# Kernel optimization log

Hardware: AMD Instinct MI355X
Metric: run time of the kernel (lower is better)

Reference implementation:

```python
import math
import jax, jax.numpy as jnp
import numpy as np

NUM_EXPERTS = 8
TOP_K = 2
HIDDEN = 1024
INTER = 4096
CAPACITY_FACTOR = 1.25
S, B = 2048, 4


def setup_inputs() -> dict:
    key = jax.random.key(0)
    k1, k2, k3, k4 = jax.random.split(key, 4)
    hidden_states = jax.random.normal(k1, (S, B, HIDDEN), dtype=jnp.float32)
    T = S * B
    logits = jax.random.normal(k2, (T, NUM_EXPERTS), dtype=jnp.float32)
    expert_affinities = jax.nn.softmax(logits, axis=-1)  # (T, E), normalized per token
    # top-k chosen experts per token (no duplicates), consistent with affinities
    _, expert_index = jax.lax.top_k(expert_affinities, TOP_K)  # (T, top_k) int32
    gate_up_proj = jax.random.normal(k3, (NUM_EXPERTS, HIDDEN, 2 * INTER), dtype=jnp.float32) * 0.02
    down_proj = jax.random.normal(k4, (NUM_EXPERTS, INTER, HIDDEN), dtype=jnp.float32) * 0.02
    return {
        "hidden_states": hidden_states,
        "expert_affinities": expert_affinities,
        "expert_index": expert_index.astype(jnp.int32),
        "gate_up_proj": gate_up_proj,
        "down_proj": down_proj,
    }


def reference(hidden_states, expert_affinities, expert_index, gate_up_proj, down_proj):
    S_, B_, H = hidden_states.shape
    T = S_ * B_
    E = expert_affinities.shape[1]
    K = expert_index.shape[1]
    # expert capacity (static, as in compute_position_in_expert)
    C = min(math.ceil(T * K * CAPACITY_FACTOR / E), T)

    x = hidden_states.reshape(T, H)

    # top_k-hot expert mask (T, E)
    expert_mask = jnp.sum(jax.nn.one_hot(expert_index, E, dtype=jnp.int32), axis=1)
    # 1-indexed position of each token within each chosen expert
    position_in_expert = jnp.cumsum(expert_mask, axis=0) * expert_mask  # (T, E)
    kept = (expert_mask > 0) & (position_in_expert <= C)  # capacity drop
    pos0 = position_in_expert - 1  # 0-indexed

    # gather per-(token, k) positions / keep flags
    pos_tk = jnp.take_along_axis(pos0, expert_index, axis=1)          # (T, K)
    kept_tk = jnp.take_along_axis(kept, expert_index, axis=1)         # (T, K)
    flat_idx = jnp.where(kept_tk, expert_index * C + pos_tk, E * C)   # dropped -> dummy slot

    # dispatch: scatter tokens into per-expert buffers (E*C [+1 dummy], H)
    src = jnp.broadcast_to(x[:, None, :], (T, K, H)).reshape(T * K, H)
    dispatched = jnp.zeros((E * C + 1, H), dtype=x.dtype).at[flat_idx.reshape(-1)].add(src)
    expert_buf = dispatched[: E * C].reshape(E, C, H)

    # grouped expert MLP (GLU): gate/up projection, SiLU gating, down projection
    gate_up = jnp.einsum("ech,ehf->ecf", expert_buf, gate_up_proj)    # (E, C, 2I)
    gate, up = jnp.split(gate_up, 2, axis=2)
    intermediate = jax.nn.silu(gate) * up                              # (E, C, I)
    expert_out = jnp.einsum("eci,eih->ech", intermediate, down_proj)   # (E, C, H)

    # combine: gather each token's expert outputs, weight by (normalized) affinities
    out_flat = jnp.concatenate(
        [expert_out.reshape(E * C, H), jnp.zeros((1, H), dtype=expert_out.dtype)], axis=0
    )
    aff_tk = jnp.take_along_axis(expert_affinities, expert_index, axis=1)  # (T, K)
    aff_tk = aff_tk / jnp.sum(aff_tk, axis=-1, keepdims=True)  # normalize_top_k_affinities
    weights = aff_tk * kept_tk.astype(aff_tk.dtype)            # dropped tokens contribute 0
    tok_out = jnp.sum(out_flat[flat_idx] * weights[..., None], axis=1)  # (T, H)
    return tok_out.reshape(S_, B_, H)
```

## Files before the change

### kernel.cpp

```cpp
#include <hip/hip_runtime.h>
#include <hip/hip_bf16.h>

#define NE 8
#define HID 1024
#define INT_ 4096
#define NTOK 8192
#define CAP 2560

typedef short short8 __attribute__((ext_vector_type(8)));
typedef float floatx4 __attribute__((ext_vector_type(4)));

__device__ __forceinline__ unsigned short f2bf(float f) {
  union { float f; unsigned int u; } v; v.f = f;
  unsigned int u = v.u;
  return (unsigned short)((u + 0x7fffu + ((u >> 16) & 1u)) >> 16);
}

__device__ __forceinline__ void gl2lds16(const void* g, void* l) {
  __builtin_amdgcn_global_load_lds(
      (const __attribute__((address_space(1))) unsigned int*)g,
      (__attribute__((address_space(3))) unsigned int*)l, 16, 0, 0);
}

__global__ void zero_f4_kernel(float4* __restrict__ p) {
  p[(size_t)blockIdx.x * 256 + threadIdx.x] = make_float4(0.f, 0.f, 0.f, 0.f);
}

__global__ void routing_kernel(const int* __restrict__ eidx, const float* __restrict__ aff,
                               int* __restrict__ tfs, float* __restrict__ sw,
                               int* __restrict__ counts) {
  __shared__ unsigned long long masks[128];
  __shared__ int ccnt[128];
  int e = blockIdx.x;
  int tid = threadIdx.x;
  int wave = tid >> 6, lane = tid & 63;

  for (int ch = wave; ch < 128; ch += 4) {
    int t = ch * 64 + lane;
    int2 pr = ((const int2*)eidx)[t];
    bool chosen = (pr.x == e) || (pr.y == e);
    unsigned long long m = __ballot(chosen);
    if (lane == 0) { masks[ch] = m; ccnt[ch] = __popcll(m); }
  }
  __syncthreads();
  if (tid == 0) {
    int run = 0;
    for (int i = 0; i < 128; ++i) { int c = ccnt[i]; ccnt[i] = run; run += c; }
    counts[e] = run < CAP ? run : CAP;
  }
  __syncthreads();
  for (int ch = wave; ch < 128; ch += 4) {
    int t = ch * 64 + lane;
    unsigned long long m = masks[ch];
    if ((m >> lane) & 1ull) {
      int pos = ccnt[ch] + __popcll(m & ((2ull << lane) - 1ull));
      if (pos <= CAP) {
        int slot = e * CAP + pos - 1;
        tfs[slot] = t;
        int2 pr = ((const int2*)eidx)[t];
        int other = (pr.x == e) ? pr.y : pr.x;
        float a0 = aff[t * NE + e], a1 = aff[t * NE + other];
        sw[slot] = a0 / (a0 + a1);
      }
    }
  }
}

__global__ void transpose_cvt_kernel(const float* __restrict__ in, unsigned short* __restrict__ out,
                                     int R, int Cc) {
  __shared__ float tile[64][33];
  int z = blockIdx.z;
  int r0 = blockIdx.y * 64, c0 = blockIdx.x * 32;
  const float* inp = in + (size_t)z * R * Cc;
  unsigned short* outp = out + (size_t)z * R * Cc;
  int tx = threadIdx.x, ty = threadIdx.y;
#pragma unroll
  for (int j = 0; j < 8; ++j) {
    int r = ty + j * 8;
    tile[r][tx] = inp[(size_t)(r0 + r) * Cc + c0 + tx];
  }
  __syncthreads();
#pragma unroll
  for (int j = 0; j < 4; ++j) {
    int c = ty + j * 8;
    ushort2 p;
    p.x = f2bf(tile[2 * tx][c]);
    p.y = f2bf(tile[2 * tx + 1][c]);
    *(ushort2*)(outp + (size_t)(c0 + c) * R + r0 + 2 * tx) = p;
  }
}

__global__ void dispatch_kernel(const float* __restrict__ x, const int* __restrict__ tfs,
                                const int* __restrict__ counts, unsigned short* __restrict__ ebuf) {
  int slot = blockIdx.x;
  int e = slot / CAP, c = slot - e * CAP;
  bool valid = c < counts[e];
  int t = valid ? tfs[slot] : 0;
  const float4* src = (const float4*)(x + (size_t)t * HID);
  ushort4* dst = (ushort4*)(ebuf + (size_t)slot * HID);
#pragma unroll
  for (int j = 0; j < 2; ++j) {
    int i = threadIdx.x + j * 128;
    ushort4 p;
    if (valid) {
      float4 v = src[i];
      p.x = f2bf(v.x); p.y = f2bf(v.y); p.z = f2bf(v.z); p.w = f2bf(v.w);
    } else {
      p.x = p.y = p.z = p.w = 0;
    }
    dst[i] = p;
  }
}

__global__ void gemm1_kernel(const unsigned short* __restrict__ ebuf,
                             const unsigned short* __restrict__ wgu,
                             const float* __restrict__ sw,
                             const int* __restrict__ counts,
                             unsigned short* __restrict__ inter) {
  int e = blockIdx.z;
  int c0 = blockIdx.y * 128;
  int f0 = blockIdx.x * 64;
  int cnt = counts[e];
  if (c0 >= cnt) return;

  __shared__ alignas(16) unsigned short smem[16384];
  unsigned short* sA = smem;
  unsigned short* sBg = smem + 8192;
  unsigned short* sBu = smem + 12288;

  int tid = threadIdx.x;
  int wave = tid >> 6, lane = tid & 63;
  int wm = (wave & 1) * 64;
  int isUp = wave >> 1;
  int lrow = lane >> 3, lch = lane & 7;
  int quad = lane >> 4, rl = lane & 15;

  const unsigned short* Ab = ebuf + ((size_t)e * CAP + c0) * HID;
  const unsigned short* Bb = wgu + ((size_t)e * 2 * INT_ + isUp * INT_ + f0) * HID;
  unsigned short* sB = isUp ? sBu : sBg;

  floatx4 acc[4][4];
#pragma unroll
  for (int i = 0; i < 4; ++i)
#pragma unroll
    for (int j = 0; j < 4; ++j) acc[i][j] = (floatx4){0.f, 0.f, 0.f, 0.f};

  for (int kk = 0; kk < HID; kk += 64) {
    __syncthreads();
#pragma unroll
    for (int i = 0; i < 4; ++i) {
      int r = wave * 32 + i * 8 + lrow;
      int gk = kk + ((lch ^ (r & 7)) << 3);
      gl2lds16(Ab + (size_t)r * HID + gk, sA + (wave * 32 + i * 8) * 64);
    }
#pragma unroll
    for (int i = 0; i < 4; ++i) {
      int r = (wave & 1) * 32 + i * 8 + lrow;
      int gk = kk + ((lch ^ (r & 7)) << 3);
      gl2lds16(Bb + (size_t)r * HID + gk, sB + ((wave & 1) * 32 + i * 8) * 64);
    }
    __syncthreads();
#pragma unroll
    for (int ks = 0; ks < 2; ++ks) {
      short8 a[4], b[4];
#pragma unroll
      for (int mi = 0; mi < 4; ++mi) {
        int r = wm + mi * 16 + rl;
        int pc = (ks * 4 + quad) ^ (r & 7);
        a[mi] = *(const short8*)(sA + r * 64 + pc * 8);
      }
#pragma unroll
      for (int ni = 0; ni < 4; ++ni) {
        int r = ni * 16 + rl;
        int pc = (ks * 4 + quad) ^ (r & 7);
        b[ni] = *(const short8*)(sB + r * 64 + pc * 8);
      }
#pragma unroll
      for (int mi = 0; mi < 4; ++mi)
#pragma unroll
        for (int ni = 0; ni < 4; ++ni)
          acc[mi][ni] = __builtin_amdgcn_mfma_f32_16x16x32_bf16(a[mi], b[ni], acc[mi][ni], 0, 0, 0);
    }
  }

  __syncthreads();
  float* gsh = (float*)smem;
  if (!isUp) {
#pragma unroll
    for (int mi = 0; mi < 4; ++mi)
#pragma unroll
      for (int ni = 0; ni < 4; ++ni)
#pragma unroll
        for (int r = 0; r < 4; ++r) {
          int row = wm + mi * 16 + quad * 4 + r;
          int col = ni * 16 + rl;
          gsh[row * 64 + col] = acc[mi][ni][r];
        }
  }
  __syncthreads();
  if (isUp) {
#pragma unroll
    for (int mi = 0; mi < 4; ++mi) {
#pragma unroll
      for (int r = 0; r < 4; ++r) {
        int row = wm + mi * 16 + quad * 4 + r;
        float w = sw[(size_t)e * CAP + c0 + row];
#pragma unroll
        for (int ni = 0; ni < 4; ++ni) {
          int col = ni * 16 + rl;
          float g = gsh[row * 64 + col];
          float u = acc[mi][ni][r];
          float s = g / (1.f + __expf(-g));
          inter[((size_t)e * CAP + c0 + row) * INT_ + f0 + col] = f2bf(s * u * w);
        }
      }
    }
  }
}

__global__ void gemm2_kernel(const unsigned short* __restrict__ inter,
                             const unsigned short* __restrict__ wd,
                             const int* __restrict__ tfs,
                             const int* __restrict__ counts,
                             float* __restrict__ out) {
  int e = blockIdx.z;
  int c0 = blockIdx.y * 128;
  int h0 = blockIdx.x * 128;
  int cnt = counts[e];
  if (c0 >= cnt) return;

  __shared__ alignas(16) unsigned short smem[16384];
  unsigned short* sA = smem;
  unsigned short* sB = smem + 8192;

  int tid = threadIdx.x;
  int wave = tid >> 6, lane = tid & 63;
  int wm = (wave & 1) * 64, wn = (wave >> 1) * 64;
  int lrow = lane >> 3, lch = lane & 7;
  int quad = lane >> 4, rl = lane & 15;

  const unsigned short* Ab = inter + ((size_t)e * CAP + c0) * INT_;
  const unsigned short* Bb = wd + ((size_t)e * HID + h0) * INT_;

  floatx4 acc[4][4];
#pragma unroll
  for (int i = 0; i < 4; ++i)
#pragma unroll
    for (int j = 0; j < 4; ++j) acc[i][j] = (floatx4){0.f, 0.f, 0.f, 0.f};

  for (int kk = 0; kk < INT_; kk += 64) {
    __syncthreads();
#pragma unroll
    for (int i = 0; i < 4; ++i) {
      int r = wave * 32 + i * 8 + lrow;
      int gk = kk + ((lch ^ (r & 7)) << 3);
      gl2lds16(Ab + (size_t)r * INT_ + gk, sA + (wave * 32 + i * 8) * 64);
      gl2lds16(Bb + (size_t)r * INT_ + gk, sB + (wave * 32 + i * 8) * 64);
    }
    __syncthreads();
#pragma unroll
    for (int ks = 0; ks < 2; ++ks) {
      short8 a[4], b[4];
#pragma unroll
      for (int mi = 0; mi < 4; ++mi) {
        int r = wm + mi * 16 + rl;
        int pc = (ks * 4 + quad) ^ (r & 7);
        a[mi] = *(const short8*)(sA + r * 64 + pc * 8);
      }
#pragma unroll
      for (int ni = 0; ni < 4; ++ni) {
        int r = wn + ni * 16 + rl;
        int pc = (ks * 4 + quad) ^ (r & 7);
        b[ni] = *(const short8*)(sB + r * 64 + pc * 8);
      }
#pragma unroll
      for (int mi = 0; mi < 4; ++mi)
#pragma unroll
        for (int ni = 0; ni < 4; ++ni)
          acc[mi][ni] = __builtin_amdgcn_mfma_f32_16x16x32_bf16(a[mi], b[ni], acc[mi][ni], 0, 0, 0);
    }
  }

#pragma unroll
  for (int mi = 0; mi < 4; ++mi) {
#pragma unroll
    for (int r = 0; r < 4; ++r) {
      int row = wm + mi * 16 + quad * 4 + r;
      int gr = c0 + row;
      if (gr < cnt) {
        int t = tfs[(size_t)e * CAP + gr];
        float* op = out + (size_t)t * HID + h0;
#pragma unroll
        for (int ni = 0; ni < 4; ++ni) atomicAdd(op + wn + ni * 16 + rl, acc[mi][ni][r]);
      }
    }
  }
}

extern "C" void kernel_launch(void* const* d_in, const int* in_sizes, int n_in,
                              void* d_out, int out_size, void* d_ws, size_t ws_size,
                              hipStream_t stream) {
  const float* x = (const float*)d_in[0];
  const float* aff = (const float*)d_in[1];
  const int* eidx = (const int*)d_in[2];
  const float* wgu_f = (const float*)d_in[3];
  const float* wd_f = (const float*)d_in[4];
  float* out = (float*)d_out;

  char* ws = (char*)d_ws;
  int* tfs = (int*)(ws + 0);
  float* sw = (float*)(ws + 81920);
  int* counts = (int*)(ws + 163840);
  unsigned short* ebuf = (unsigned short*)(ws + 262144);
  unsigned short* wgu = (unsigned short*)(ws + 42205184);
  unsigned short* wd = (unsigned short*)(ws + 176422912);
  unsigned short* inter = (unsigned short*)(ws + 243531776);

  zero_f4_kernel<<<8192, 256, 0, stream>>>((float4*)out);
  routing_kernel<<<NE, 256, 0, stream>>>(eidx, aff, tfs, sw, counts);
  transpose_cvt_kernel<<<dim3(256, 16, NE), dim3(32, 8), 0, stream>>>(wgu_f, wgu, 1024, 8192);
  transpose_cvt_kernel<<<dim3(32, 64, NE), dim3(32, 8), 0, stream>>>(wd_f, wd, 4096, 1024);
  dispatch_kernel<<<NE * CAP, 128, 0, stream>>>(x, tfs, counts, ebuf);
  gemm1_kernel<<<dim3(64, 20, NE), 256, 0, stream>>>(ebuf, wgu, sw, counts, inter);
  gemm2_kernel<<<dim3(8, 20, NE), 256, 0, stream>>>(inter, wd, tfs, counts, out);
}
```

Measured before the change: 1.087 ms.

## Replace atomic scatter-add with per-slot store plus combine gather; widen weight transpose

The down-projection GEMM now writes each expert-slot output to a dense fp32 buffer instead of atomically adding into the token output. A new combine kernel gathers each token's two slot rows and applies the normalized affinity weights. This removes the output zeroing pass and the atomic contention, and moves the routing weight out of the gate/up epilogue. The weight transpose-and-convert kernel now loads float4 values, converts to bf16 before staging in shared memory, and stores ushort4 with 64x64 tiles. The cost is an extra ~84MB intermediate buffer written and read back through global memory.

```diff
diff --git a/kernel.cpp b/kernel.cpp
--- a/kernel.cpp
+++ b/kernel.cpp
@@ -22,13 +22,9 @@
       (__attribute__((address_space(3))) unsigned int*)l, 16, 0, 0);
 }
 
-__global__ void zero_f4_kernel(float4* __restrict__ p) {
-  p[(size_t)blockIdx.x * 256 + threadIdx.x] = make_float4(0.f, 0.f, 0.f, 0.f);
-}
-
-__global__ void routing_kernel(const int* __restrict__ eidx, const float* __restrict__ aff,
-                               int* __restrict__ tfs, float* __restrict__ sw,
-                               int* __restrict__ counts) {
+__global__ void routing_kernel(const int* __restrict__ eidx,
+                               int* __restrict__ tfs,
+                               int* __restrict__ counts, int* __restrict__ slots) {
   __shared__ unsigned long long masks[128];
   __shared__ int ccnt[128];
   int e = blockIdx.x;
@@ -54,13 +50,14 @@
     unsigned long long m = masks[ch];
     if ((m >> lane) & 1ull) {
       int pos = ccnt[ch] + __popcll(m & ((2ull << lane) - 1ull));
+      int2 pr = ((const int2*)eidx)[t];
+      int kk = (pr.x == e) ? 0 : 1;
       if (pos <= CAP) {
         int slot = e * CAP + pos - 1;
         tfs[slot] = t;
-        int2 pr = ((const int2*)eidx)[t];
-        int other = (pr.x == e) ? pr.y : pr.x;
-        float a0 = aff[t * NE + e], a1 = aff[t * NE + other];
-        sw[slot] = a0 / (a0 + a1);
+        slots[2 * t + kk] = slot;
+      } else {
+        slots[2 * t + kk] = -1;
       }
     }
   }
@@ -68,25 +65,31 @@
 
 __global__ void transpose_cvt_kernel(const float* __restrict__ in, unsigned short* __restrict__ out,
                                      int R, int Cc) {
-  __shared__ float tile[64][33];
+  __shared__ unsigned short tile[64 * 66];
   int z = blockIdx.z;
-  int r0 = blockIdx.y * 64, c0 = blockIdx.x * 32;
+  int r0 = blockIdx.y * 64, c0 = blockIdx.x * 64;
   const float* inp = in + (size_t)z * R * Cc;
   unsigned short* outp = out + (size_t)z * R * Cc;
-  int tx = threadIdx.x, ty = threadIdx.y;
-#pragma unroll
-  for (int j = 0; j < 8; ++j) {
-    int r = ty + j * 8;
-    tile[r][tx] = inp[(size_t)(r0 + r) * Cc + c0 + tx];
-  }
-  __syncthreads();
+  int tx = threadIdx.x & 15, ty = threadIdx.x >> 4;
 #pragma unroll
   for (int j = 0; j < 4; ++j) {
-    int c = ty + j * 8;
-    ushort2 p;
-    p.x = f2bf(tile[2 * tx][c]);
-    p.y = f2bf(tile[2 * tx + 1][c]);
-    *(ushort2*)(outp + (size_t)(c0 + c) * R + r0 + 2 * tx) = p;
+    int r = ty + j * 16;
+    float4 v = *(const float4*)(inp + (size_t)(r0 + r) * Cc + c0 + 4 * tx);
+    tile[r * 66 + 4 * tx + 0] = f2bf(v.x);
+    tile[r * 66 + 4 * tx + 1] = f2bf(v.y);
+    tile[r * 66 + 4 * tx + 2] = f2bf(v.z);
+    tile[r * 66 + 4 * tx + 3] = f2bf(v.w);
+  }
+  __syncthreads();
+#pragma unroll
+  for (int j = 0; j < 4; ++j) {
+    int c = ty + j * 16;
+    ushort4 p;
+    p.x = tile[(4 * tx + 0) * 66 + c];
+    p.y = tile[(4 * tx + 1) * 66 + c];
+    p.z = tile[(4 * tx + 2) * 66 + c];
+    p.w = tile[(4 * tx + 3) * 66 + c];
+    *(ushort4*)(outp + (size_t)(c0 + c) * R + r0 + 4 * tx) = p;
   }
 }
 
@@ -114,7 +117,6 @@
 
 __global__ void gemm1_kernel(const unsigned short* __restrict__ ebuf,
                              const unsigned short* __restrict__ wgu,
-                             const float* __restrict__ sw,
                              const int* __restrict__ counts,
                              unsigned short* __restrict__ inter) {
   int e = blockIdx.z;
@@ -204,14 +206,13 @@
 #pragma unroll
       for (int r = 0; r < 4; ++r) {
         int row = wm + mi * 16 + quad * 4 + r;
-        float w = sw[(size_t)e * CAP + c0 + row];
 #pragma unroll
         for (int ni = 0; ni < 4; ++ni) {
           int col = ni * 16 + rl;
           float g = gsh[row * 64 + col];
           float u = acc[mi][ni][r];
           float s = g / (1.f + __expf(-g));
-          inter[((size_t)e * CAP + c0 + row) * INT_ + f0 + col] = f2bf(s * u * w);
+          inter[((size_t)e * CAP + c0 + row) * INT_ + f0 + col] = f2bf(s * u);
         }
       }
     }
@@ -220,9 +221,8 @@
 
 __global__ void gemm2_kernel(const unsigned short* __restrict__ inter,
                              const unsigned short* __restrict__ wd,
-                             const int* __restrict__ tfs,
                              const int* __restrict__ counts,
-                             float* __restrict__ out) {
+                             float* __restrict__ eout) {
   int e = blockIdx.z;
   int c0 = blockIdx.y * 128;
   int h0 = blockIdx.x * 128;
@@ -286,15 +286,34 @@
 #pragma unroll
     for (int r = 0; r < 4; ++r) {
       int row = wm + mi * 16 + quad * 4 + r;
-      int gr = c0 + row;
-      if (gr < cnt) {
-        int t = tfs[(size_t)e * CAP + gr];
-        float* op = out + (size_t)t * HID + h0;
-#pragma unroll
-        for (int ni = 0; ni < 4; ++ni) atomicAdd(op + wn + ni * 16 + rl, acc[mi][ni][r]);
-      }
-    }
-  }
+      float* op = eout + ((size_t)e * CAP + c0 + row) * HID + h0;
+#pragma unroll
+      for (int ni = 0; ni < 4; ++ni) op[wn + ni * 16 + rl] = acc[mi][ni][r];
+    }
+  }
+}
+
+__global__ void combine_kernel(const float4* __restrict__ eout, const int* __restrict__ slots,
+                               const float* __restrict__ aff, const int* __restrict__ eidx,
+                               float4* __restrict__ out) {
+  int t = blockIdx.x;
+  int i = threadIdx.x;
+  int s0 = slots[2 * t], s1 = slots[2 * t + 1];
+  int e0 = eidx[2 * t], e1 = eidx[2 * t + 1];
+  float a0 = aff[t * NE + e0], a1 = aff[t * NE + e1];
+  float inv = 1.f / (a0 + a1);
+  float w0 = (s0 >= 0) ? a0 * inv : 0.f;
+  float w1 = (s1 >= 0) ? a1 * inv : 0.f;
+  int p0 = (s0 >= 0) ? s0 : 0;
+  int p1 = (s1 >= 0) ? s1 : 0;
+  float4 v0 = eout[(size_t)p0 * 256 + i];
+  float4 v1 = eout[(size_t)p1 * 256 + i];
+  float4 r;
+  r.x = w0 * v0.x + w1 * v1.x;
+  r.y = w0 * v0.y + w1 * v1.y;
+  r.z = w0 * v0.z + w1 * v1.z;
+  r.w = w0 * v0.w + w1 * v1.w;
+  out[(size_t)t * 256 + i] = r;
 }
 
 extern "C" void kernel_launch(void* const* d_in, const int* in_sizes, int n_in,
@@ -309,18 +328,19 @@
 
   char* ws = (char*)d_ws;
   int* tfs = (int*)(ws + 0);
-  float* sw = (float*)(ws + 81920);
   int* counts = (int*)(ws + 163840);
+  int* slots = (int*)(ws + 196608);
   unsigned short* ebuf = (unsigned short*)(ws + 262144);
   unsigned short* wgu = (unsigned short*)(ws + 42205184);
   unsigned short* wd = (unsigned short*)(ws + 176422912);
   unsigned short* inter = (unsigned short*)(ws + 243531776);
-
-  zero_f4_kernel<<<8192, 256, 0, stream>>>((float4*)out);
-  routing_kernel<<<NE, 256, 0, stream>>>(eidx, aff, tfs, sw, counts);
-  transpose_cvt_kernel<<<dim3(256, 16, NE), dim3(32, 8), 0, stream>>>(wgu_f, wgu, 1024, 8192);
-  transpose_cvt_kernel<<<dim3(32, 64, NE), dim3(32, 8), 0, stream>>>(wd_f, wd, 4096, 1024);
+  float* eout = (float*)(ws + 42205184);
+
+  routing_kernel<<<NE, 256, 0, stream>>>(eidx, tfs, counts, slots);
+  transpose_cvt_kernel<<<dim3(128, 16, NE), 256, 0, stream>>>(wgu_f, wgu, 1024, 8192);
+  transpose_cvt_kernel<<<dim3(16, 64, NE), 256, 0, stream>>>(wd_f, wd, 4096, 1024);
   dispatch_kernel<<<NE * CAP, 128, 0, stream>>>(x, tfs, counts, ebuf);
-  gemm1_kernel<<<dim3(64, 20, NE), 256, 0, stream>>>(ebuf, wgu, sw, counts, inter);
-  gemm2_kernel<<<dim3(8, 20, NE), 256, 0, stream>>>(inter, wd, tfs, counts, out);
-}
+  gemm1_kernel<<<dim3(64, 20, NE), 256, 0, stream>>>(ebuf, wgu, counts, inter);
+  gemm2_kernel<<<dim3(8, 20, NE), 256, 0, stream>>>(inter, wd, counts, eout);
+  combine_kernel<<<NTOK, 256, 0, stream>>>((const float4*)eout, slots, aff, eidx, (float4*)out);
+}
```

Result: faster. 1.037 ms (-4.6%).
